# Performance work log

Hardware: AMD Instinct MI355X
Metric: run time of the kernel (lower is better)

The kernel has to match this reference:

```python
import jax, jax.numpy as jnp
import numpy as np

EMBED_DIM = 1024
NUM_HEADS = 16
HEAD_DIM = EMBED_DIM // NUM_HEADS
BATCH = 2
SEQ = 2048


def setup_inputs() -> dict:
    key = jax.random.key(0)
    ks = jax.random.split(key, 9)
    scale = 1.0 / np.sqrt(EMBED_DIM)
    return {
        "inputs": jax.random.normal(ks[0], (BATCH, SEQ, EMBED_DIM), jnp.float32),
        "Wq": jax.random.normal(ks[1], (EMBED_DIM, EMBED_DIM), jnp.float32) * scale,
        "bq": jnp.zeros((EMBED_DIM,), jnp.float32),
        "Wk": jax.random.normal(ks[2], (EMBED_DIM, EMBED_DIM), jnp.float32) * scale,
        "bk": jnp.zeros((EMBED_DIM,), jnp.float32),
        "Wv": jax.random.normal(ks[3], (EMBED_DIM, EMBED_DIM), jnp.float32) * scale,
        "bv": jnp.zeros((EMBED_DIM,), jnp.float32),
        "Wo": jax.random.normal(ks[4], (EMBED_DIM, EMBED_DIM), jnp.float32) * scale,
        "bo": jnp.zeros((EMBED_DIM,), jnp.float32),
    }


def reference(inputs, Wq, bq, Wk, bk, Wv, bv, Wo, bo):
    B, S, D = inputs.shape
    H, Dh = NUM_HEADS, HEAD_DIM

    def split_heads(x):  # [B,S,D] -> [B,H,S,Dh]
        return x.reshape(B, S, H, Dh).transpose(0, 2, 1, 3)

    Q = split_heads(inputs @ Wq + bq)
    K = split_heads(inputs @ Wk + bk)
    V = split_heads(inputs @ Wv + bv)

    # naive full-score attention, faithful to the original
    scores = jnp.einsum("bhqd,bhkd->bhqk", Q, K) / jnp.sqrt(jnp.float32(Dh))
    weights = jax.nn.softmax(scores, axis=-1)
    out = jnp.einsum("bhqk,bhkd->bhqd", weights, V)

    concat = out.transpose(0, 2, 1, 3).reshape(B, S, D)
    return concat @ Wo + bo
```

## Files before the change

### kernel.cpp

```cpp
#include <hip/hip_runtime.h>

#define EMBED 1024
#define NHEAD 16
#define HDIM  64
#define BATCH 2
#define SEQ   2048
#define MTOK  (BATCH * SEQ)
#define QSCALE 0.1803368801f

typedef __bf16 bf16x8 __attribute__((ext_vector_type(8)));
typedef float  f32x4  __attribute__((ext_vector_type(4)));

__device__ __forceinline__ unsigned short f2bf(float f) {
  return (unsigned short)((__float_as_uint(f) + 0x8000u) >> 16);
}
__device__ __forceinline__ unsigned int pkbf(float a, float b) {
  unsigned int ua = __float_as_uint(a) + 0x8000u;
  unsigned int ub = __float_as_uint(b) + 0x8000u;
  return __builtin_amdgcn_perm(ub, ua, 0x07060302u);
}

__device__ __forceinline__ void gload_lds16(const unsigned short* g, unsigned short* l) {
  __builtin_amdgcn_global_load_lds((__attribute__((address_space(1))) void*)g,
                                   (__attribute__((address_space(3))) void*)l, 16, 0, 0);
}

__global__ void cast_bf16_k(const float* __restrict__ src,
                            unsigned short* __restrict__ dst, int n4) {
  int i = blockIdx.x * blockDim.x + threadIdx.x;
  if (i < n4) {
    float4 f = reinterpret_cast<const float4*>(src)[i];
    uint2 u = make_uint2(pkbf(f.x, f.y), pkbf(f.z, f.w));
    reinterpret_cast<uint2*>(dst)[i] = u;
  }
}

__global__ __launch_bounds__(256)
void transpose_cast4_k(const float* __restrict__ s0, const float* __restrict__ s1,
                       const float* __restrict__ s2, const float* __restrict__ s3,
                       unsigned short* __restrict__ d0, unsigned short* __restrict__ d1,
                       unsigned short* __restrict__ d2, unsigned short* __restrict__ d3) {
  const float* s; unsigned short* d;
  switch (blockIdx.z) {
    case 0: s = s0; d = d0; break;
    case 1: s = s1; d = d1; break;
    case 2: s = s2; d = d2; break;
    default: s = s3; d = d3; break;
  }
  __shared__ unsigned short T[64][65];
  const int k0 = blockIdx.x * 64, n0 = blockIdx.y * 64;
  for (int i = threadIdx.x; i < 4096; i += 256) {
    int r = i >> 6, c = i & 63;
    T[c][r] = f2bf(s[(size_t)(k0 + r) * EMBED + n0 + c]);
  }
  __syncthreads();
  for (int i = threadIdx.x; i < 4096; i += 256) {
    int r = i >> 6, c = i & 63;
    d[(size_t)(n0 + r) * EMBED + k0 + c] = T[r][c];
  }
}

__global__ __launch_bounds__(256)
void vtrans_k(const unsigned short* __restrict__ Vn,
              unsigned short* __restrict__ Vt) {
  __shared__ unsigned short T[64][65];
  const int s0 = blockIdx.x * 64;
  const size_t base = (size_t)blockIdx.y * SEQ * HDIM;
  for (int i = threadIdx.x; i < 1024; i += 256) {
    int r = i >> 4, c4 = (i & 15) * 4;
    ushort4 v = *reinterpret_cast<const ushort4*>(&Vn[base + (size_t)(s0 + r) * HDIM + c4]);
    T[c4][r] = v.x; T[c4 + 1][r] = v.y; T[c4 + 2][r] = v.z; T[c4 + 3][r] = v.w;
  }
  __syncthreads();
  for (int i = threadIdx.x; i < 1024; i += 256) {
    int r = i >> 4, c4 = (i & 15) * 4;
    ushort4 v;
    v.x = T[r][c4]; v.y = T[r][c4 + 1]; v.z = T[r][c4 + 2]; v.w = T[r][c4 + 3];
    *reinterpret_cast<ushort4*>(&Vt[base + (size_t)r * SEQ + s0 + c4]) = v;
  }
}

template<int MODE, int BM>
__global__ __launch_bounds__(256, 2)
void gemm_k(const unsigned short* __restrict__ A,
            const unsigned short* __restrict__ Bt,
            const float* __restrict__ b0, const float* __restrict__ b1,
            const float* __restrict__ b2,
            unsigned short* __restrict__ oQ, unsigned short* __restrict__ oK,
            unsigned short* __restrict__ oV, float* __restrict__ oF) {
  constexpr int MI = BM / 32;
  __shared__ unsigned short As[BM][64];
  __shared__ unsigned short Bs[128][64];
  const int tid = threadIdx.x, lane = tid & 63, wave = tid >> 6;
  const int lr = lane & 15, quad = lane >> 4;
  const int wm = (wave >> 1) * (BM / 2), wn = (wave & 1) * 64;
  const int row0 = blockIdx.x * BM, col0 = blockIdx.y * 128;
  const int srow = lane >> 3, sc = lane & 7;
  const int sw0 = (quad ^ (lr & 7)) * 8;
  const int sw1 = ((quad ^ 4) ^ (lr & 7)) * 8;

  const f32x4 fz = {0.f, 0.f, 0.f, 0.f};
  f32x4 acc[MI][4];
#pragma unroll
  for (int i = 0; i < MI; ++i)
#pragma unroll
    for (int j = 0; j < 4; ++j) acc[i][j] = fz;

  for (int k0 = 0; k0 < EMBED; k0 += 64) {
#pragma unroll
    for (int g = 0; g < BM / 32; ++g) {
      int rbase = wave * (BM / 4) + g * 8;
      int row = rbase + srow;
      gload_lds16(&A[(size_t)(row0 + row) * EMBED + k0 + ((sc ^ (row & 7)) * 8)],
                  &As[rbase][0]);
    }
#pragma unroll
    for (int g = 0; g < 4; ++g) {
      int rbase = wave * 32 + g * 8;
      int row = rbase + srow;
      gload_lds16(&Bt[(size_t)(col0 + row) * EMBED + k0 + ((sc ^ (row & 7)) * 8)],
                  &Bs[rbase][0]);
    }
    __syncthreads();
#pragma unroll
    for (int kk = 0; kk < 64; kk += 32) {
      const int so = (kk == 0) ? sw0 : sw1;
      bf16x8 af[MI], bv[4];
#pragma unroll
      for (int i = 0; i < MI; ++i)
        af[i] = *reinterpret_cast<const bf16x8*>(&As[wm + i * 16 + lr][so]);
#pragma unroll
      for (int j = 0; j < 4; ++j)
        bv[j] = *reinterpret_cast<const bf16x8*>(&Bs[wn + j * 16 + lr][so]);
#pragma unroll
      for (int i = 0; i < MI; ++i)
#pragma unroll
        for (int j = 0; j < 4; ++j)
          acc[i][j] = __builtin_amdgcn_mfma_f32_16x16x32_bf16(af[i], bv[j],
                                                              acc[i][j], 0, 0, 0);
    }
    __syncthreads();
  }

#pragma unroll
  for (int i = 0; i < MI; ++i) {
#pragma unroll
    for (int j = 0; j < 4; ++j) {
      const int col = col0 + wn + j * 16 + lr;
      if (MODE == 1) {
        const float bb = b0[col];
#pragma unroll
        for (int r = 0; r < 4; ++r) {
          const int row = row0 + wm + i * 16 + quad * 4 + r;
          oF[((size_t)row << 10) + col] = acc[i][j][r] + bb;
        }
      } else {
        const int which = col >> 10, cn = col & 1023;
        const float bb = (which == 0 ? b0 : which == 1 ? b1 : b2)[cn];
        unsigned short* o = (which == 0 ? oQ : which == 1 ? oK : oV);
        const float sscale = (which == 0) ? QSCALE : 1.0f;
        const int h = cn >> 6, dd = cn & 63;
#pragma unroll
        for (int r = 0; r < 4; ++r) {
          const int row = row0 + wm + i * 16 + quad * 4 + r;
          const int b = row >> 11, ss = row & (SEQ - 1);
          o[((((size_t)b * NHEAD + h) * SEQ + ss) << 6) + dd] =
              f2bf((acc[i][j][r] + bb) * sscale);
        }
      }
    }
  }
}

__global__ __launch_bounds__(256, 4)
void attn_k(const unsigned short* __restrict__ Qb,
            const unsigned short* __restrict__ Kb,
            const unsigned short* __restrict__ Vt,
            unsigned short* __restrict__ Ctx) {
  __shared__ unsigned short Qs[64][64];
  __shared__ unsigned short Ks[64][64];
  __shared__ unsigned short Vs[64][64];
  __shared__ unsigned short Ps[64][64];
  const int tid = threadIdx.x, lane = tid & 63, wave = tid >> 6;
  const int lr = lane & 15, quad = lane >> 4;
  const int qt = blockIdx.x, bh = blockIdx.y;
  const size_t base = (size_t)bh * SEQ * HDIM;
  const int srow = lane >> 3, sc = lane & 7;
  const int sw0 = (quad ^ (lr & 7)) * 8;
  const int sw1 = ((quad ^ 4) ^ (lr & 7)) * 8;

#pragma unroll
  for (int g = 0; g < 2; ++g) {
    int rbase = wave * 16 + g * 8;
    int row = rbase + srow;
    gload_lds16(&Qb[base + (size_t)(qt * 64 + row) * HDIM + ((sc ^ (row & 7)) * 8)],
                &Qs[rbase][0]);
    gload_lds16(&Kb[base + (size_t)row * HDIM + ((sc ^ (row & 7)) * 8)], &Ks[rbase][0]);
    gload_lds16(&Vt[base + (size_t)row * SEQ + ((sc ^ (row & 7)) * 8)], &Vs[rbase][0]);
  }
  __syncthreads();

  const bf16x8 qf0 = *reinterpret_cast<const bf16x8*>(&Qs[wave * 16 + lr][sw0]);
  const bf16x8 qf1 = *reinterpret_cast<const bf16x8*>(&Qs[wave * 16 + lr][sw1]);

  float l_part = 0.f;
  const f32x4 fz = {0.f, 0.f, 0.f, 0.f};
  f32x4 oacc[4] = {fz, fz, fz, fz};

  for (int kt = 0;;) {
    f32x4 sc4[4];
#pragma unroll
    for (int nt = 0; nt < 4; ++nt) {
      bf16x8 kf0 = *reinterpret_cast<const bf16x8*>(&Ks[nt * 16 + lr][sw0]);
      bf16x8 kf1 = *reinterpret_cast<const bf16x8*>(&Ks[nt * 16 + lr][sw1]);
      f32x4 a = __builtin_amdgcn_mfma_f32_16x16x32_bf16(kf0, qf0, fz, 0, 0, 0);
      sc4[nt] = __builtin_amdgcn_mfma_f32_16x16x32_bf16(kf1, qf1, a, 0, 0, 0);
    }

#pragma unroll
    for (int nt = 0; nt < 4; ++nt) {
      float p0 = __builtin_amdgcn_exp2f(sc4[nt][0]);
      float p1 = __builtin_amdgcn_exp2f(sc4[nt][1]);
      float p2 = __builtin_amdgcn_exp2f(sc4[nt][2]);
      float p3 = __builtin_amdgcn_exp2f(sc4[nt][3]);
      l_part += (p0 + p1) + (p2 + p3);
      const int pc = (nt * 2 + (quad >> 1)) ^ (lr & 7);
      *reinterpret_cast<uint2*>(&Ps[wave * 16 + lr][pc * 8 + (quad & 1) * 4]) =
          make_uint2(pkbf(p0, p1), pkbf(p2, p3));
    }

    __threadfence_block();

    const bf16x8 pa0 = *reinterpret_cast<const bf16x8*>(&Ps[wave * 16 + lr][sw0]);
    const bf16x8 pa1 = *reinterpret_cast<const bf16x8*>(&Ps[wave * 16 + lr][sw1]);
#pragma unroll
    for (int d = 0; d < 4; ++d) {
      bf16x8 vb0 = *reinterpret_cast<const bf16x8*>(&Vs[d * 16 + lr][sw0]);
      bf16x8 vb1 = *reinterpret_cast<const bf16x8*>(&Vs[d * 16 + lr][sw1]);
      oacc[d] = __builtin_amdgcn_mfma_f32_16x16x32_bf16(pa0, vb0, oacc[d], 0, 0, 0);
      oacc[d] = __builtin_amdgcn_mfma_f32_16x16x32_bf16(pa1, vb1, oacc[d], 0, 0, 0);
    }

    if (++kt == SEQ / 64) break;
    __syncthreads();
#pragma unroll
    for (int g = 0; g < 2; ++g) {
      int rbase = wave * 16 + g * 8;
      int row = rbase + srow;
      gload_lds16(&Kb[base + (size_t)(kt * 64 + row) * HDIM + ((sc ^ (row & 7)) * 8)],
                  &Ks[rbase][0]);
      gload_lds16(&Vt[base + (size_t)row * SEQ + kt * 64 + ((sc ^ (row & 7)) * 8)],
                  &Vs[rbase][0]);
    }
    __syncthreads();
  }

  l_part += __shfl_xor(l_part, 16);
  l_part += __shfl_xor(l_part, 32);

  const int b = bh >> 4, h = bh & 15;
  float linv[4];
#pragma unroll
  for (int r = 0; r < 4; ++r) linv[r] = 1.0f / __shfl(l_part, quad * 4 + r);
#pragma unroll
  for (int d = 0; d < 4; ++d)
#pragma unroll
    for (int r = 0; r < 4; ++r) {
      const int q = qt * 64 + wave * 16 + quad * 4 + r;
      Ctx[(((size_t)b * SEQ + q) << 10) + h * 64 + d * 16 + lr] =
          f2bf(oacc[d][r] * linv[r]);
    }
}

extern "C" void kernel_launch(void* const* d_in, const int* in_sizes, int n_in,
                              void* d_out, int out_size, void* d_ws, size_t ws_size,
                              hipStream_t stream) {
  const float* X  = (const float*)d_in[0];
  const float* Wq = (const float*)d_in[1];
  const float* bq = (const float*)d_in[2];
  const float* Wk = (const float*)d_in[3];
  const float* bk = (const float*)d_in[4];
  const float* Wv = (const float*)d_in[5];
  const float* bv = (const float*)d_in[6];
  const float* Wo = (const float*)d_in[7];
  const float* bo = (const float*)d_in[8];

  unsigned short* ws = (unsigned short*)d_ws;
  const size_t M1 = (size_t)1024 * 1024;
  unsigned short* Xbf = ws;
  unsigned short* WqT = ws + 4 * M1;
  unsigned short* WkT = ws + 5 * M1;
  unsigned short* WvT = ws + 6 * M1;
  unsigned short* WoT = ws + 7 * M1;
  unsigned short* Qb  = ws + 8 * M1;
  unsigned short* Kb  = ws + 12 * M1;
  unsigned short* Vn  = ws + 16 * M1;
  unsigned short* Vt  = Xbf;
  unsigned short* Ctx = Vn;

  cast_bf16_k<<<4096, 256, 0, stream>>>(X, Xbf, MTOK * EMBED / 4);
  transpose_cast4_k<<<dim3(16, 16, 4), 256, 0, stream>>>(Wq, Wk, Wv, Wo,
                                                         WqT, WkT, WvT, WoT);

  gemm_k<0, 128><<<dim3(MTOK / 128, 3072 / 128), 256, 0, stream>>>(
      Xbf, WqT, bq, bk, bv, Qb, Kb, Vn, nullptr);

  vtrans_k<<<dim3(SEQ / 64, BATCH * NHEAD), 256, 0, stream>>>(Vn, Vt);

  attn_k<<<dim3(SEQ / 64, BATCH * NHEAD), 256, 0, stream>>>(Qb, Kb, Vt, Ctx);

  gemm_k<1, 64><<<dim3(MTOK / 64, EMBED / 128), 256, 0, stream>>>(
      Ctx, WoT, bo, nullptr, nullptr, nullptr, nullptr, nullptr, (float*)d_out);
}
```

Baseline: 201.6 us.

## Fuse V transpose into QKV GEMM epilogue, share Q/P LDS, reorder grids

```diff
diff --git a/kernel.cpp b/kernel.cpp
--- a/kernel.cpp
+++ b/kernel.cpp
@@ -60,41 +60,20 @@
   }
 }
 
-__global__ __launch_bounds__(256)
-void vtrans_k(const unsigned short* __restrict__ Vn,
-              unsigned short* __restrict__ Vt) {
-  __shared__ unsigned short T[64][65];
-  const int s0 = blockIdx.x * 64;
-  const size_t base = (size_t)blockIdx.y * SEQ * HDIM;
-  for (int i = threadIdx.x; i < 1024; i += 256) {
-    int r = i >> 4, c4 = (i & 15) * 4;
-    ushort4 v = *reinterpret_cast<const ushort4*>(&Vn[base + (size_t)(s0 + r) * HDIM + c4]);
-    T[c4][r] = v.x; T[c4 + 1][r] = v.y; T[c4 + 2][r] = v.z; T[c4 + 3][r] = v.w;
-  }
-  __syncthreads();
-  for (int i = threadIdx.x; i < 1024; i += 256) {
-    int r = i >> 4, c4 = (i & 15) * 4;
-    ushort4 v;
-    v.x = T[r][c4]; v.y = T[r][c4 + 1]; v.z = T[r][c4 + 2]; v.w = T[r][c4 + 3];
-    *reinterpret_cast<ushort4*>(&Vt[base + (size_t)r * SEQ + s0 + c4]) = v;
-  }
-}
-
 template<int MODE, int BM>
-__global__ __launch_bounds__(256, 2)
-void gemm_k(const unsigned short* __restrict__ A,
-            const unsigned short* __restrict__ Bt,
-            const float* __restrict__ b0, const float* __restrict__ b1,
-            const float* __restrict__ b2,
-            unsigned short* __restrict__ oQ, unsigned short* __restrict__ oK,
-            unsigned short* __restrict__ oV, float* __restrict__ oF) {
+__global__ void gemm_k(const unsigned short* __restrict__ A,
+                       const unsigned short* __restrict__ Bt,
+                       const float* __restrict__ b0, const float* __restrict__ b1,
+                       const float* __restrict__ b2,
+                       unsigned short* __restrict__ oQ, unsigned short* __restrict__ oK,
+                       unsigned short* __restrict__ oV, float* __restrict__ oF) {
   constexpr int MI = BM / 32;
   __shared__ unsigned short As[BM][64];
   __shared__ unsigned short Bs[128][64];
   const int tid = threadIdx.x, lane = tid & 63, wave = tid >> 6;
   const int lr = lane & 15, quad = lane >> 4;
   const int wm = (wave >> 1) * (BM / 2), wn = (wave & 1) * 64;
-  const int row0 = blockIdx.x * BM, col0 = blockIdx.y * 128;
+  const int col0 = blockIdx.x * 128, row0 = blockIdx.y * BM;
   const int srow = lane >> 3, sc = lane & 7;
   const int sw0 = (quad ^ (lr & 7)) * 8;
   const int sw1 = ((quad ^ 4) ^ (lr & 7)) * 8;
@@ -157,33 +136,37 @@
       } else {
         const int which = col >> 10, cn = col & 1023;
         const float bb = (which == 0 ? b0 : which == 1 ? b1 : b2)[cn];
-        unsigned short* o = (which == 0 ? oQ : which == 1 ? oK : oV);
         const float sscale = (which == 0) ? QSCALE : 1.0f;
         const int h = cn >> 6, dd = cn & 63;
 #pragma unroll
         for (int r = 0; r < 4; ++r) {
           const int row = row0 + wm + i * 16 + quad * 4 + r;
           const int b = row >> 11, ss = row & (SEQ - 1);
-          o[((((size_t)b * NHEAD + h) * SEQ + ss) << 6) + dd] =
-              f2bf((acc[i][j][r] + bb) * sscale);
+          const float v = (acc[i][j][r] + bb) * sscale;
+          if (which == 0) {
+            oQ[((((size_t)b * NHEAD + h) * SEQ + ss) << 6) + dd] = f2bf(v);
+          } else if (which == 1) {
+            oK[((((size_t)b * NHEAD + h) * SEQ + ss) << 6) + dd] = f2bf(v);
+          } else {
+            oV[(((size_t)b * NHEAD + h) * HDIM + dd) * SEQ + ss] = f2bf(v);
+          }
         }
       }
     }
   }
 }
 
-__global__ __launch_bounds__(256, 4)
+__global__ __launch_bounds__(256, 6)
 void attn_k(const unsigned short* __restrict__ Qb,
             const unsigned short* __restrict__ Kb,
             const unsigned short* __restrict__ Vt,
             unsigned short* __restrict__ Ctx) {
-  __shared__ unsigned short Qs[64][64];
+  __shared__ unsigned short QPs[64][64];
   __shared__ unsigned short Ks[64][64];
   __shared__ unsigned short Vs[64][64];
-  __shared__ unsigned short Ps[64][64];
   const int tid = threadIdx.x, lane = tid & 63, wave = tid >> 6;
   const int lr = lane & 15, quad = lane >> 4;
-  const int qt = blockIdx.x, bh = blockIdx.y;
+  const int bh = blockIdx.x, qt = blockIdx.y;
   const size_t base = (size_t)bh * SEQ * HDIM;
   const int srow = lane >> 3, sc = lane & 7;
   const int sw0 = (quad ^ (lr & 7)) * 8;
@@ -194,14 +177,15 @@
     int rbase = wave * 16 + g * 8;
     int row = rbase + srow;
     gload_lds16(&Qb[base + (size_t)(qt * 64 + row) * HDIM + ((sc ^ (row & 7)) * 8)],
-                &Qs[rbase][0]);
+                &QPs[rbase][0]);
     gload_lds16(&Kb[base + (size_t)row * HDIM + ((sc ^ (row & 7)) * 8)], &Ks[rbase][0]);
     gload_lds16(&Vt[base + (size_t)row * SEQ + ((sc ^ (row & 7)) * 8)], &Vs[rbase][0]);
   }
   __syncthreads();
 
-  const bf16x8 qf0 = *reinterpret_cast<const bf16x8*>(&Qs[wave * 16 + lr][sw0]);
-  const bf16x8 qf1 = *reinterpret_cast<const bf16x8*>(&Qs[wave * 16 + lr][sw1]);
+  const bf16x8 qf0 = *reinterpret_cast<const bf16x8*>(&QPs[wave * 16 + lr][sw0]);
+  const bf16x8 qf1 = *reinterpret_cast<const bf16x8*>(&QPs[wave * 16 + lr][sw1]);
+  __threadfence_block();
 
   float l_part = 0.f;
   const f32x4 fz = {0.f, 0.f, 0.f, 0.f};
@@ -225,14 +209,14 @@
       float p3 = __builtin_amdgcn_exp2f(sc4[nt][3]);
       l_part += (p0 + p1) + (p2 + p3);
       const int pc = (nt * 2 + (quad >> 1)) ^ (lr & 7);
-      *reinterpret_cast<uint2*>(&Ps[wave * 16 + lr][pc * 8 + (quad & 1) * 4]) =
+      *reinterpret_cast<uint2*>(&QPs[wave * 16 + lr][pc * 8 + (quad & 1) * 4]) =
           make_uint2(pkbf(p0, p1), pkbf(p2, p3));
     }
 
     __threadfence_block();
 
-    const bf16x8 pa0 = *reinterpret_cast<const bf16x8*>(&Ps[wave * 16 + lr][sw0]);
-    const bf16x8 pa1 = *reinterpret_cast<const bf16x8*>(&Ps[wave * 16 + lr][sw1]);
+    const bf16x8 pa0 = *reinterpret_cast<const bf16x8*>(&QPs[wave * 16 + lr][sw0]);
+    const bf16x8 pa1 = *reinterpret_cast<const bf16x8*>(&QPs[wave * 16 + lr][sw1]);
 #pragma unroll
     for (int d = 0; d < 4; ++d) {
       bf16x8 vb0 = *reinterpret_cast<const bf16x8*>(&Vs[d * 16 + lr][sw0]);
@@ -294,21 +278,18 @@
   unsigned short* WoT = ws + 7 * M1;
   unsigned short* Qb  = ws + 8 * M1;
   unsigned short* Kb  = ws + 12 * M1;
-  unsigned short* Vn  = ws + 16 * M1;
-  unsigned short* Vt  = Xbf;
-  unsigned short* Ctx = Vn;
+  unsigned short* Vt  = ws + 16 * M1;
+  unsigned short* Ctx = ws + 20 * M1;
 
   cast_bf16_k<<<4096, 256, 0, stream>>>(X, Xbf, MTOK * EMBED / 4);
   transpose_cast4_k<<<dim3(16, 16, 4), 256, 0, stream>>>(Wq, Wk, Wv, Wo,
                                                          WqT, WkT, WvT, WoT);
 
-  gemm_k<0, 128><<<dim3(MTOK / 128, 3072 / 128), 256, 0, stream>>>(
-      Xbf, WqT, bq, bk, bv, Qb, Kb, Vn, nullptr);
-
-  vtrans_k<<<dim3(SEQ / 64, BATCH * NHEAD), 256, 0, stream>>>(Vn, Vt);
-
-  attn_k<<<dim3(SEQ / 64, BATCH * NHEAD), 256, 0, stream>>>(Qb, Kb, Vt, Ctx);
-
-  gemm_k<1, 64><<<dim3(MTOK / 64, EMBED / 128), 256, 0, stream>>>(
+  gemm_k<0, 128><<<dim3(3072 / 128, MTOK / 128), 256, 0, stream>>>(
+      Xbf, WqT, bq, bk, bv, Qb, Kb, Vt, nullptr);
+
+  attn_k<<<dim3(BATCH * NHEAD, SEQ / 64), 256, 0, stream>>>(Qb, Kb, Vt, Ctx);
+
+  gemm_k<1, 64><<<dim3(EMBED / 128, MTOK / 64), 256, 0, stream>>>(
       Ctx, WoT, bo, nullptr, nullptr, nullptr, nullptr, nullptr, (float*)d_out);
 }
```

After: 204.1 us. Within noise of the previous version (+1.2%).
